# Performance work log

Hardware: AMD Instinct MI355X
Metric: run time of the kernel (lower is better)

Reference implementation:

```python
import jax, jax.numpy as jnp
import numpy as np

H = 256      # HIDDEN_DIM
F_IN = 16    # input_dim
B = 512
S = 168      # encoder sequence length
T = 24       # PRED_LEN


def _lstm_cell(x, h, c, w_ih, w_hh, b):
    # torch gate order: i, f, g, o
    g = x @ w_ih.T + h @ w_hh.T + b
    i, f, gg, o = jnp.split(g, 4, axis=-1)
    c_new = jax.nn.sigmoid(f) * c + jax.nn.sigmoid(i) * jnp.tanh(gg)
    h_new = jax.nn.sigmoid(o) * jnp.tanh(c_new)
    return h_new, c_new


def _lstm_layer(x, w_ih, w_hh, b):
    # x: [S, B, in] -> outputs [S, B, H], final (h, c)
    Bv, Hv = x.shape[1], w_hh.shape[1]
    init = (jnp.zeros((Bv, Hv), x.dtype), jnp.zeros((Bv, Hv), x.dtype))
    def step(carry, xt):
        h, c = _lstm_cell(xt, carry[0], carry[1], w_ih, w_hh, b)
        return (h, c), h
    (h, c), ys = jax.lax.scan(step, init, x)
    return ys, h, c


def setup_inputs() -> dict:
    key = jax.random.key(0)
    ks = jax.random.split(key, 24)
    s = 1.0 / np.sqrt(H)
    u = lambda k, shape: jax.random.uniform(k, shape, jnp.float32, -s, s)
    inp = {}
    inp['src'] = jax.random.normal(ks[0], (B, S, F_IN), jnp.float32)
    # encoder LSTM (2 layers); biases b_ih + b_hh fused into one vector
    inp['enc_w_ih0'] = u(ks[1], (4 * H, F_IN))
    inp['enc_w_hh0'] = u(ks[2], (4 * H, H))
    inp['enc_b0'] = u(ks[3], (4 * H,))
    inp['enc_w_ih1'] = u(ks[4], (4 * H, H))
    inp['enc_w_hh1'] = u(ks[5], (4 * H, H))
    inp['enc_b1'] = u(ks[6], (4 * H,))
    # decoder LSTM (2 layers), input_size = 1 + H
    inp['dec_w_ih0'] = u(ks[7], (4 * H, 1 + H))
    inp['dec_w_hh0'] = u(ks[8], (4 * H, H))
    inp['dec_b0'] = u(ks[9], (4 * H,))
    inp['dec_w_ih1'] = u(ks[10], (4 * H, H))
    inp['dec_w_hh1'] = u(ks[11], (4 * H, H))
    inp['dec_b1'] = u(ks[12], (4 * H,))
    # attention: Linear(2H -> H), v: Linear(H -> 1, no bias), position bias
    inp['attn_w'] = u(ks[13], (H, 2 * H))
    inp['attn_b'] = u(ks[14], (H,))
    inp['attn_v'] = u(ks[15], (H,))
    inp['pos_bias'] = jax.random.normal(ks[16], (H,), jnp.float32)
    # fc_out: Linear(H -> 1)
    inp['fc_w'] = u(ks[17], (1, H))
    inp['fc_b'] = u(ks[18], (1,))
    return inp


def reference(src, enc_w_ih0, enc_w_hh0, enc_b0, enc_w_ih1, enc_w_hh1, enc_b1,
              dec_w_ih0, dec_w_hh0, dec_b0, dec_w_ih1, dec_w_hh1, dec_b1,
              attn_w, attn_b, attn_v, pos_bias, fc_w, fc_b):
    x = jnp.transpose(src, (1, 0, 2))  # [S, B, F]
    y0, _, _ = _lstm_layer(x, enc_w_ih0, enc_w_hh0, enc_b0)
    enc_out_t, h1e, c1e = _lstm_layer(y0, enc_w_ih1, enc_w_hh1, enc_b1)
    # also need final state of layer 0 for decoder init
    h0e, c0e = y0[-1], None
    # recompute layer-0 final cell state: rerun scan carry output
    # (cheap alternative: _lstm_layer returns (ys, h, c); reuse it)
    _, h0e, c0e = _lstm_layer(x, enc_w_ih0, enc_w_hh0, enc_b0)
    enc_out = jnp.transpose(enc_out_t, (1, 0, 2))  # [B, S, H]

    We, Wd = attn_w[:, :H], attn_w[:, H:]
    enc_proj = jnp.einsum('bsh,gh->bsg', enc_out, We)  # precomputed encoder projection
    dec_in0 = src[:, -1, -1:]  # [B, 1]

    def dec_step(carry, t):
        h0, c0, h1, c1, dec_in = carry
        # additive attention using top-layer decoder hidden
        e = jnp.tanh(enc_proj + (h1 @ Wd.T + attn_b)[:, None, :])
        e = e + pos_bias[None, None, :] * (t / 24.0)
        w = jax.nn.softmax(e @ attn_v, axis=1)              # [B, S]
        ctx = jnp.einsum('bs,bsh->bh', w, enc_out)          # [B, H]
        x0 = jnp.concatenate([dec_in, ctx], axis=1)          # [B, 1+H]
        h0n, c0n = _lstm_cell(x0, h0, c0, dec_w_ih0, dec_w_hh0, dec_b0)
        h1n, c1n = _lstm_cell(h0n, h1, c1, dec_w_ih1, dec_w_hh1, dec_b1)
        pred = h1n @ fc_w.T + fc_b                           # [B, 1]
        # NOTE: the gated blend of decoder_output in the source is dead code
        # (the blended tensor is never used), so it is omitted here.
        return (h0n, c0n, h1n, c1n, pred), pred

    ts = jnp.arange(T, dtype=src.dtype)
    _, preds = jax.lax.scan(dec_step, (h0e, c0e, h1e, c1e, dec_in0), ts)
    return jnp.transpose(preds, (1, 0, 2))  # [B, T, 1]
```

## Files before the change

kernel.cpp:

```cpp
#include <hip/hip_runtime.h>
#include <hip/hip_fp16.h>
#include <math.h>

#define BB 512
#define HH 256
#define SS 168
#define TT 24
#define NBLK 256
#define NTHR 512
typedef unsigned long long ull;
typedef unsigned short u16;
#define BH 131072ull

#define O_Y0  0ull
#define O_H1  262144ull
#define O_H0  524288ull
#define O_CTX 786432ull
#define O_W0  933888ull
#define O_W1  1261568ull
#define O_WP  2834432ull
#define O_WDT 2835456ull
#define O_BP  2900992ull
#define O_E16 2905088ull
#define O_P16 13915136ull

typedef float f32x4 __attribute__((ext_vector_type(4)));
typedef float v2f __attribute__((ext_vector_type(2)));
typedef unsigned int ru4 __attribute__((ext_vector_type(4)));

__device__ __forceinline__ float sigf(float x) { return 1.f / (1.f + expf(-x)); }

#define AR __ATOMIC_RELAXED
#define SCA __HIP_MEMORY_SCOPE_AGENT
__device__ __forceinline__ int aLd(const int* p) { return __hip_atomic_load(p, AR, SCA); }

__device__ __forceinline__ float2 ld2(const float* p) {
  ull raw = __hip_atomic_load((const ull*)p, AR, SCA);
  float2 v; v.x = __uint_as_float((unsigned)raw); v.y = __uint_as_float((unsigned)(raw >> 32));
  return v;
}
__device__ __forceinline__ float ld1(const float* p) {
  unsigned raw = __hip_atomic_load((const unsigned*)p, AR, SCA);
  return __uint_as_float(raw);
}
__device__ __forceinline__ void st1(float* p, float v) {
  __hip_atomic_store((unsigned*)p, __float_as_uint(v), AR, SCA);
}
__device__ __forceinline__ void sth(__half* p, __half v) {
  __hip_atomic_store((unsigned short*)p, __half_as_ushort(v), AR, SCA);
}
__device__ __forceinline__ void stu(unsigned* p, unsigned v) {
  __hip_atomic_store(p, v, AR, SCA);
}

__device__ __forceinline__ void ld_h2(const float* p, v2f& a) {
  asm volatile("global_load_dwordx2 %0, %1, off sc0 sc1"
               : "=&v"(a) : "v"(p) : "memory");
}
__device__ __forceinline__ void ld_w2(const u16* ph, const u16* pl, ru4& h, ru4& l) {
  asm volatile("global_load_dwordx4 %0, %2, off\n\t"
               "global_load_dwordx4 %1, %3, off"
               : "=&v"(h), "=&v"(l) : "v"(ph), "v"(pl) : "memory");
}
#define VMW(n) asm volatile("s_waitcnt vmcnt(" #n ")" ::: "memory")

#define MFMA(d, a, b) asm volatile("v_mfma_f32_16x16x32_bf16 %0, %1, %2, %0" \
                                   : "+v"(d) : "v"(a), "v"(b))
#define TOUCH(x) asm volatile("" : "+v"(x))

#define SSTR 16
__device__ __forceinline__ void arrive_slot(int* slot, int val) {
  asm volatile("s_waitcnt vmcnt(0)" ::: "memory");
  __syncthreads();
  if (threadIdx.x == 0) __hip_atomic_store(slot, val, AR, SCA);
}
__device__ __forceinline__ void wait_slots(const int* base, int n, int tgt) {
  if (threadIdx.x < 64) {
    const int lane = threadIdx.x;
    const int* p = base + lane * SSTR;
    for (;;) {
      const int ok = (lane >= n) || (aLd(p) >= tgt);
      if (__all(ok)) break;
      __builtin_amdgcn_s_sleep(1);
    }
  }
  __syncthreads();
}
__device__ __forceinline__ void wait_slots2(const int* a, int na, const int* b, int nb, int tgt) {
  if (threadIdx.x < 64) {
    const int lane = threadIdx.x;
    const int* p = (lane < na) ? (a + lane * SSTR)
                 : (lane < na + nb) ? (b + (lane - na) * SSTR) : (const int*)nullptr;
    for (;;) {
      const int ok = (p == nullptr) || (aLd(p) >= tgt);
      if (__all(ok)) break;
      __builtin_amdgcn_s_sleep(1);
    }
  }
  __syncthreads();
}

struct SMT {
  union {
    struct { unsigned WsH[128][20]; unsigned WsL[128][20]; float Ht[32][36]; } m;
    struct { float As[32][65];  float Bs[32][65]; } g;
    struct { float h1s[256], qs[256], vs[256], sc[192], ctxs[1024], sred[4]; } at;
  };
};

__device__ __forceinline__ void fma16(float acc[4][4], const float4 hv, const float4 wv) {
  acc[0][0] += hv.x * wv.x; acc[0][1] += hv.x * wv.y; acc[0][2] += hv.x * wv.z; acc[0][3] += hv.x * wv.w;
  acc[1][0] += hv.y * wv.x; acc[1][1] += hv.y * wv.y; acc[1][2] += hv.y * wv.z; acc[1][3] += hv.y * wv.w;
  acc[2][0] += hv.z * wv.x; acc[2][1] += hv.z * wv.y; acc[2][2] += hv.z * wv.z; acc[2][3] += hv.z * wv.w;
  acc[3][0] += hv.w * wv.x; acc[3][1] += hv.w * wv.y; acc[3][2] += hv.w * wv.z; acc[3][3] += hv.w * wv.w;
}

__device__ __forceinline__ unsigned rne16(unsigned u) {
  return (u + 0x7fffu + ((u >> 16) & 1u)) >> 16;
}
__device__ __forceinline__ void split8v(const f32x4 a, const f32x4 b, ru4& hi, ru4& lo) {
#pragma unroll
  for (int j = 0; j < 4; j++) {
    const float x = (j < 2) ? a[2 * j] : b[2 * j - 4];
    const float y = (j < 2) ? a[2 * j + 1] : b[2 * j - 3];
    const unsigned hx = rne16(__float_as_uint(x)), hy = rne16(__float_as_uint(y));
    const float rx = x - __uint_as_float(hx << 16);
    const float ry = y - __uint_as_float(hy << 16);
    hi[j] = (hx & 0xffffu) | (hy << 16);
    lo[j] = (rne16(__float_as_uint(rx)) & 0xffffu) | (rne16(__float_as_uint(ry)) << 16);
  }
}

__device__ __forceinline__ void comp_mfma(SMT& sm, int wq, int w1, int l15, int l4,
                                          f32x4 acc[2])
{
  const int hr = w1 * 16 + l15;
  const f32x4 hv0 = *(const f32x4*)&sm.m.Ht[hr][l4 * 8];
  const f32x4 hv1 = *(const f32x4*)&sm.m.Ht[hr][l4 * 8 + 4];
  ru4 bhi, blo;
  split8v(hv0, hv1, bhi, blo);
  asm volatile("s_nop 1" : "+v"(bhi), "+v"(blo));
#pragma unroll
  for (int g = 0; g < 2; g++) {
    const int cr = wq * 32 + g * 16 + l15;
    ru4 ah = *(const ru4*)&sm.m.WsH[cr][l4 * 4];
    ru4 al = *(const ru4*)&sm.m.WsL[cr][l4 * 4];
    MFMA(acc[g], ah, bhi);
    MFMA(acc[g], ah, blo);
    MFMA(acc[g], al, bhi);
  }
}

#define STW(wh, wl) do { \
  *(ru4*)&sm.m.WsH[cgt][kt * 4] = (wh); \
  *(ru4*)&sm.m.WsL[cgt][kt * 4] = (wl); } while (0)
#define STH(a) do { \
  sm.m.Ht[r][p2 * 2] = (a)[0]; sm.m.Ht[r][p2 * 2 + 1] = (a)[1]; } while (0)

__device__ void gemm_pipe(const u16* wbh, const u16* wbl,
                          const float* hb0, const float* hb1,
                          int NC, int nc0, f32x4 acc[2], SMT& sm,
                          int wq, int w1, int l15, int l4)
{
  const int tid = threadIdx.x;
  const int r = tid & 31, p2 = tid >> 5;
  const int cgt = tid & 127, kt = tid >> 7;
  const float* h1p = hb1 - (ull)nc0 * 32;
#define HBk(k) (((k) < nc0) ? (hb0 + (k) * 32) : (h1p + (k) * 32))
  ru4 wh0, wl0, wh1, wl1, wh2, wl2, wh3, wl3;
  v2f h0, h1, h2, h3;
  ld_w2(wbh,      wbl,      wh0, wl0);
  ld_h2(HBk(0), h0);
  ld_w2(wbh + 32, wbl + 32, wh1, wl1);
  ld_h2(HBk(1), h1);
  ld_h2(HBk(2), h2);
  for (int c = 0; c < NC; c += 4) {
    VMW(4);
    STW(wh0, wl0); STH(h0);
    __syncthreads();
    ld_w2(wbh + (c + 2) * 32, wbl + (c + 2) * 32, wh2, wl2);
    ld_h2(HBk(c + 3), h3);
    comp_mfma(sm, wq, w1, l15, l4, acc);
    __syncthreads();
    VMW(4);
    STW(wh1, wl1); STH(h1);
    __syncthreads();
    ld_w2(wbh + (c + 3) * 32, wbl + (c + 3) * 32, wh3, wl3);
    ld_h2(HBk(c + 4), h0);
    comp_mfma(sm, wq, w1, l15, l4, acc);
    __syncthreads();
    VMW(4);
    STW(wh2, wl2); STH(h2);
    __syncthreads();
    ld_w2(wbh + (c + 4) * 32, wbl + (c + 4) * 32, wh0, wl0);
    ld_h2(HBk(c + 5), h1);
    comp_mfma(sm, wq, w1, l15, l4, acc);
    __syncthreads();
    VMW(4);
    STW(wh3, wl3); STH(h3);
    __syncthreads();
    ld_w2(wbh + (c + 5) * 32, wbl + (c + 5) * 32, wh1, wl1);
    ld_h2(HBk(c + 6), h2);
    comp_mfma(sm, wq, w1, l15, l4, acc);
    __syncthreads();
  }
  asm volatile("s_waitcnt vmcnt(0)" ::: "memory");
  asm volatile("s_nop 7\n\ts_nop 7" : "+v"(acc[0]), "+v"(acc[1]));
#undef HBk
}

__device__ __forceinline__ void lstm_epi2(f32x4 acc[2], float cR[2], int row, int ubase, int l4,
                                          float* hout, __half* e16, int sstep)
{
#pragma unroll
  for (int g = 0; g < 2; g++) {
    const int u = ubase + g * 4 + l4;
    const float iv = sigf(acc[g][0]), fv = sigf(acc[g][1]);
    const float gv = tanhf(acc[g][2]), ov = sigf(acc[g][3]);
    const float cn = fv * cR[g] + iv * gv;
    cR[g] = cn;
    const float hn = ov * tanhf(cn);
    st1(hout + (ull)row * 256 + u, hn);
    if (e16) sth(e16 + ((ull)row * SS + sstep) * 256 + u, __float2half(hn));
  }
}

__device__ void attn_fc(int row, int t, int slot, const float* h1r, const float* wdT,
                        const float* attn_b, const float* attn_v,
                        const __half* P16, const __half* E16,
                        const float* fc_w, const float* fc_b,
                        float* ctxb, float* out, SMT& sm)
{
  const int tid = threadIdx.x;
  __syncthreads();
  if (tid < 128) {
    float2 v = ld2(h1r + (ull)slot * BH + (ull)row * 256 + tid * 2);
    sm.at.h1s[tid * 2] = v.x; sm.at.h1s[tid * 2 + 1] = v.y;
  }
  __syncthreads();
  if (t >= 1 && tid < 64) {
    float a = 0.f;
#pragma unroll
    for (int j = 0; j < 4; j++) a += sm.at.h1s[tid + 64 * j] * fc_w[tid + 64 * j];
#pragma unroll
    for (int m = 32; m >= 1; m >>= 1) a += __shfl_xor(a, m, 64);
    if (tid == 0) {
      const float p = a + fc_b[0];
      out[(ull)row * TT + (t - 1)] = p;
      st1(ctxb + (ull)row * 288 + 256, p);
    }
  }
  if (t >= TT) return;
  if (tid < 256) {
    float qv = attn_b[tid];
    for (int k = 0; k < 256; k += 4) {
      qv += sm.at.h1s[k]     * wdT[(ull)(k)     * 256 + tid];
      qv += sm.at.h1s[k + 1] * wdT[(ull)(k + 1) * 256 + tid];
      qv += sm.at.h1s[k + 2] * wdT[(ull)(k + 2) * 256 + tid];
      qv += sm.at.h1s[k + 3] * wdT[(ull)(k + 3) * 256 + tid];
    }
    sm.at.qs[tid] = qv;
    sm.at.vs[tid] = attn_v[tid];
  }
  __syncthreads();
  const int wv = tid >> 6, lane = tid & 63;
  for (int s = wv; s < SS; s += 8) {
    const __half2* Pr = (const __half2*)(P16 + ((ull)row * SS + s) * 256);
    float a = 0.f;
#pragma unroll
    for (int jj = 0; jj < 2; jj++) {
      const int i2 = lane + 64 * jj;
      const float2 pv = __half22float2(Pr[i2]);
      const int g0 = i2 * 2;
      a += sm.at.vs[g0] * tanhf(pv.x + sm.at.qs[g0]);
      a += sm.at.vs[g0 + 1] * tanhf(pv.y + sm.at.qs[g0 + 1]);
    }
#pragma unroll
    for (int m = 32; m >= 1; m >>= 1) a += __shfl_xor(a, m, 64);
    if (lane == 0) sm.at.sc[s] = a;
  }
  __syncthreads();
  if (tid < 64) {
    float m = -1e30f;
    for (int i = tid; i < SS; i += 64) m = fmaxf(m, sm.at.sc[i]);
#pragma unroll
    for (int mm = 32; mm >= 1; mm >>= 1) m = fmaxf(m, __shfl_xor(m, mm, 64));
    if (tid == 0) sm.at.sred[0] = m;
  }
  __syncthreads();
  const float smax = sm.at.sred[0];
  if (tid < SS) sm.at.sc[tid] = expf(sm.at.sc[tid] - smax);
  __syncthreads();
  if (tid < 64) {
    float ssum = 0.f;
    for (int i = tid; i < SS; i += 64) ssum += sm.at.sc[i];
#pragma unroll
    for (int mm = 32; mm >= 1; mm >>= 1) ssum += __shfl_xor(ssum, mm, 64);
    if (tid == 0) sm.at.sred[1] = ssum;
  }
  __syncthreads();
  const float rinv = 1.f / sm.at.sred[1];
  const int u2 = tid & 127, sh = tid >> 7;
  float cx = 0.f, cy = 0.f;
  for (int s = sh * 42; s < sh * 42 + 42; s++) {
    const float w = sm.at.sc[s] * rinv;
    const float2 ev = __half22float2(*(const __half2*)(E16 + ((ull)row * SS + s) * 256 + u2 * 2));
    cx += w * ev.x; cy += w * ev.y;
  }
  sm.at.ctxs[sh * 256 + u2 * 2] = cx;
  sm.at.ctxs[sh * 256 + u2 * 2 + 1] = cy;
  __syncthreads();
  if (tid < 256)
    st1(ctxb + (ull)row * 288 + tid,
        sm.at.ctxs[tid] + sm.at.ctxs[256 + tid] + sm.at.ctxs[512 + tid] + sm.at.ctxs[768 + tid]);
}

__device__ void proj_tile(const __half* E16, const float* attn_w, __half* P16,
                          int m0, int n0, SMT& sm)
{
  const int tid = threadIdx.x;
  const bool act = tid < 256;
  const int mq = tid & 15, nq = (tid >> 4) & 15;
  const int li = tid & 63, kq = (tid >> 6) & 3;
  float acc[4][4] = {{0.f}};
  for (int k0 = 0; k0 < 256; k0 += 32) {
    if (act) {
      float4 raw = *(const float4*)(E16 + (ull)(m0 + li) * 256 + k0 + kq * 8);
      const __half* hp = (const __half*)&raw;
#pragma unroll
      for (int i = 0; i < 8; i++) sm.g.As[kq * 8 + i][li] = __half2float(hp[i]);
      const float* gb = attn_w + (ull)(n0 + li) * 512 + k0 + kq * 8;
      const float4 v0 = *(const float4*)gb, v1 = *(const float4*)(gb + 4);
      sm.g.Bs[kq * 8 + 0][li] = v0.x; sm.g.Bs[kq * 8 + 1][li] = v0.y;
      sm.g.Bs[kq * 8 + 2][li] = v0.z; sm.g.Bs[kq * 8 + 3][li] = v0.w;
      sm.g.Bs[kq * 8 + 4][li] = v1.x; sm.g.Bs[kq * 8 + 5][li] = v1.y;
      sm.g.Bs[kq * 8 + 6][li] = v1.z; sm.g.Bs[kq * 8 + 7][li] = v1.w;
    }
    __syncthreads();
    if (act) {
#pragma unroll 8
      for (int kk = 0; kk < 32; kk++) {
        const float4 a4 = *(const float4*)&sm.g.As[kk][mq * 4];
        const float4 b4 = *(const float4*)&sm.g.Bs[kk][nq * 4];
        fma16(acc, a4, b4);
      }
    }
    __syncthreads();
  }
  if (act) {
#pragma unroll
    for (int i = 0; i < 4; i++) {
      const int m = m0 + mq * 4 + i;
#pragma unroll
      for (int j = 0; j < 2; j++) {
        __half2 h2; h2.x = __float2half(acc[i][j * 2]); h2.y = __float2half(acc[i][j * 2 + 1]);
        stu((unsigned*)(P16 + (ull)m * 256 + n0 + nq * 4) + j, *(unsigned*)&h2);
      }
    }
  }
}

__global__ __launch_bounds__(512, 1) void seq2seq_pipe(
    const float* __restrict__ src,
    const float* __restrict__ attn_w, const float* __restrict__ attn_b,
    const float* __restrict__ attn_v,
    const float* __restrict__ fc_w, const float* __restrict__ fc_b,
    float* __restrict__ out, int* __restrict__ ib)
{
  __shared__ SMT sm;
  const int blk = blockIdx.x;
  const int tid = threadIdx.x;
  float* fb = (float*)ib + 65536;
  float* y0r  = fb + O_Y0;
  float* h1r  = fb + O_H1;
  float* h0r  = fb + O_H0;
  float* zb   = h0r + BH;
  float* ctxb = fb + O_CTX;
  const u16* whi0 = (const u16*)(fb + O_W0);
  const u16* wlo0 = whi0 + 1024ull * 320;
  const u16* whi1 = (const u16*)(fb + O_W1);
  const u16* wlo1 = whi1 + 1024ull * 512;
  const u16* dhi0 = whi1 + 2ull * 1024 * 512;
  const u16* dlo0 = whi1 + 3ull * 1024 * 512;
  const u16* dhi1 = whi1 + 4ull * 1024 * 512;
  const u16* dlo1 = whi1 + 5ull * 1024 * 512;
  const float* wp  = fb + O_WP;
  const float* wdT = fb + O_WDT;
  const float* bp  = fb + O_BP;
  __half* E16 = (__half*)(fb + O_E16);
  __half* P16 = (__half*)(fb + O_P16);
  const int g = blk >> 5, m = blk & 31;
  const int rowg = g * 64;
  int* gf = ib + g * 4096;
  int* f_e0 = gf;
  int* f_e1 = gf + 256;
  int* f_pr = gf + 512;
  int* f_a  = gf + 1024;
  int* f_h0 = gf + 1536;
  int* f_h1 = gf + 1792;

  const int lm = (m < 16) ? m : (m - 16);
  const int rh = lm & 1, gi = lm >> 1;
  const int row0 = rowg + rh * 32;
  const int gc0 = gi * 128;
  const int w = tid >> 6;
  const int l15 = tid & 15, l4 = (tid >> 4) & 3;
  const int w1 = w & 1, wq = w >> 1;
  const int gcw = gc0 + wq * 32;
  const int myrow = row0 + w1 * 16 + l15;
  const int ubase = gcw >> 2;
  const int r = tid & 31;
  const int cgt = tid & 127, kt = tid >> 7;

  int* my_enc_slot = (m < 16 ? f_e0 : f_e1) + (rh * 8 + gi) * SSTR;
  const int* e0h = f_e0 + rh * 8 * SSTR;
  const int* e1h = f_e1 + rh * 8 * SSTR;

  float cReg[2] = {0.f, 0.f};

  for (int t = 0; t <= SS; t++) {
    if (t) wait_slots2(e0h, 8, e1h, 8, t);
    if (m < 16) {
      if (t < SS) {
        f32x4 acc[2];
#pragma unroll
        for (int gg = 0; gg < 2; gg++) {
          acc[gg] = *(const f32x4*)(bp + gcw + gg * 16 + l4 * 4);
          TOUCH(acc[gg]);
        }
        {
          ru4 wxh, wxl;
          ld_w2(whi0 + (ull)(gc0 + cgt) * 320 + kt * 8,
                wlo0 + (ull)(gc0 + cgt) * 320 + kt * 8, wxh, wxl);
          VMW(0);
          *(ru4*)&sm.m.WsH[cgt][kt * 4] = wxh;
          *(ru4*)&sm.m.WsL[cgt][kt * 4] = wxl;
          const int f = tid >> 5;
          sm.m.Ht[r][f]      = src[((ull)(row0 + r) * SS + t) * 16 + f];
          sm.m.Ht[r][f + 16] = 0.f;
          __syncthreads();
          comp_mfma(sm, wq, w1, l15, l4, acc);
          __syncthreads();
        }
        const float* ysrc = (t == 0) ? zb : (y0r + (ull)((t + 1) & 1) * BH);
        const float* hb0 = ysrc + (ull)(row0 + r) * 256 + (tid >> 5) * 2;
        gemm_pipe(whi0 + (ull)(gc0 + cgt) * 320 + 32 + kt * 8,
                  wlo0 + (ull)(gc0 + cgt) * 320 + 32 + kt * 8,
                  hb0, hb0, 8, 8, acc, sm, wq, w1, l15, l4);
        lstm_epi2(acc, cReg, myrow, ubase, l4, y0r + (ull)(t & 1) * BH, nullptr, 0);
      }
    } else {
      if (t >= 1) {
        const int s = t - 1;
        f32x4 acc[2];
#pragma unroll
        for (int gg = 0; gg < 2; gg++) {
          acc[gg] = *(const f32x4*)(bp + 1024 + gcw + gg * 16 + l4 * 4);
          TOUCH(acc[gg]);
        }
        const float* ysrc = y0r + (ull)(s & 1) * BH;
        const float* hsrc = (s == 0) ? zb : (h1r + (ull)((s + 1) & 1) * BH);
        const float* hb0 = ysrc + (ull)(row0 + r) * 256 + (tid >> 5) * 2;
        const float* hb1 = hsrc + (ull)(row0 + r) * 256 + (tid >> 5) * 2;
        gemm_pipe(whi1 + (ull)(gc0 + cgt) * 512 + kt * 8,
                  wlo1 + (ull)(gc0 + cgt) * 512 + kt * 8,
                  hb0, hb1, 16, 8, acc, sm, wq, w1, l15, l4);
        lstm_epi2(acc, cReg, myrow, ubase, l4, h1r + (ull)(s & 1) * BH, E16, s);
      }
    }
    arrive_slot(my_enc_slot, t + 1);
  }

  wait_slots(f_e1, 16, SS + 1);
  {
    const int em0 = rowg * SS;
    for (int tau = m; tau < 672; tau += 32)
      proj_tile(E16, attn_w, P16, em0 + (tau >> 2) * 64, (tau & 3) * 64, sm);
  }
  arrive_slot(f_pr + m * SSTR, 1);

  for (int t = 0; t <= TT; t++) {
    if (t == 0) wait_slots(f_pr, 32, 1);
    else wait_slots(f_h1, 16, t);
    const int slot = (t + 1) & 1;
    attn_fc(rowg + 2 * m,     t, slot, h1r, wdT, attn_b, attn_v, P16, E16, fc_w, fc_b, ctxb, out, sm);
    attn_fc(rowg + 2 * m + 1, t, slot, h1r, wdT, attn_b, attn_v, P16, E16, fc_w, fc_b, ctxb, out, sm);
    if (t == TT) break;
    arrive_slot(f_a + m * SSTR, t + 1);
    if (m < 16) {
      wait_slots(f_a, 32, t + 1);
      if (t) wait_slots(f_h0, 16, t);
      f32x4 acc[2];
#pragma unroll
      for (int gg = 0; gg < 2; gg++) {
        acc[gg] = *(const f32x4*)(bp + 2048 + gcw + gg * 16 + l4 * 4);
        TOUCH(acc[gg]);
      }
      const float* h0src = (t == 0) ? (y0r + BH) : (h0r + (ull)((t + 1) & 1) * BH);
      const float* hb0 = ctxb + (ull)(row0 + r) * 288 + (tid >> 5) * 2;
      const float* hb1 = h0src + (ull)(row0 + r) * 256 + (tid >> 5) * 2;
      gemm_pipe(dhi0 + (ull)(gc0 + cgt) * 512 + kt * 8,
                dlo0 + (ull)(gc0 + cgt) * 512 + kt * 8,
                hb0, hb1, 16, 8, acc, sm, wq, w1, l15, l4);
      const float p = ld1(ctxb + (ull)myrow * 288 + 256);
#pragma unroll
      for (int gg = 0; gg < 2; gg++) {
        const f32x4 wpv = *(const f32x4*)(wp + gcw + gg * 16 + l4 * 4);
        acc[gg] = acc[gg] + wpv * p;
      }
      lstm_epi2(acc, cReg, myrow, ubase, l4, h0r + (ull)(t & 1) * BH, nullptr, 0);
      arrive_slot(f_h0 + m * SSTR, t + 1);
    } else {
      wait_slots(f_h0, 16, t + 1);
      if (t) wait_slots(f_h1, 16, t);
      f32x4 acc[2];
#pragma unroll
      for (int gg = 0; gg < 2; gg++) {
        acc[gg] = *(const f32x4*)(bp + 3072 + gcw + gg * 16 + l4 * 4);
        TOUCH(acc[gg]);
      }
      const float* hb0 = h0r + (ull)(t & 1) * BH + (ull)(row0 + r) * 256 + (tid >> 5) * 2;
      const float* hb1 = h1r + (ull)((t + 1) & 1) * BH + (ull)(row0 + r) * 256 + (tid >> 5) * 2;
      gemm_pipe(dhi1 + (ull)(gc0 + cgt) * 512 + kt * 8,
                dlo1 + (ull)(gc0 + cgt) * 512 + kt * 8,
                hb0, hb1, 16, 8, acc, sm, wq, w1, l15, l4);
      lstm_epi2(acc, cReg, myrow, ubase, l4, h1r + (ull)(t & 1) * BH, nullptr, 0);
      arrive_slot(f_h1 + (m - 16) * SSTR, t + 1);
    }
  }
}

__device__ __forceinline__ void split_store(float v, u16* hi, u16* lo, ull i) {
  const unsigned u = __float_as_uint(v);
  const unsigned hb = (u + 0x7fffu + ((u >> 16) & 1u)) >> 16;
  const float rr = v - __uint_as_float(hb << 16);
  const unsigned ur = __float_as_uint(rr);
  const unsigned lb = (ur + 0x7fffu + ((ur >> 16) & 1u)) >> 16;
  hi[i] = (u16)hb; lo[i] = (u16)lb;
}

__global__ void init_all(
    const float* __restrict__ src,
    const float* __restrict__ ewih0, const float* __restrict__ ewhh0, const float* __restrict__ eb0,
    const float* __restrict__ ewih1, const float* __restrict__ ewhh1, const float* __restrict__ eb1,
    const float* __restrict__ dwih0, const float* __restrict__ dwhh0, const float* __restrict__ db0,
    const float* __restrict__ dwih1, const float* __restrict__ dwhh1, const float* __restrict__ db1,
    const float* __restrict__ attn_w, int* __restrict__ ib)
{
  const int gid = blockIdx.x * 256 + threadIdx.x;
  const int NG = 1024 * 256;
  float* fb = (float*)ib + 65536;
  u16* whi0 = (u16*)(fb + O_W0);
  u16* wlo0 = whi0 + 1024ull * 320;
  u16* whi1 = (u16*)(fb + O_W1);
  u16* wlo1 = whi1 + 1024ull * 512;
  u16* dhi0 = whi1 + 2ull * 1024 * 512;
  u16* dlo0 = whi1 + 3ull * 1024 * 512;
  u16* dhi1 = whi1 + 4ull * 1024 * 512;
  u16* dlo1 = whi1 + 5ull * 1024 * 512;
  float* wpd = fb + O_WP;

  for (int i = gid; i < 32768; i += NG) ib[i] = 0;
  for (int i = gid; i < (int)BH; i += NG) fb[O_H0 + BH + i] = 0.f;
  for (int i = gid; i < 1024 * 320; i += NG) {
    const int cg = i / 320, k = i - cg * 320, j = (cg & 3) * 256 + (cg >> 2);
    float v = 0.f;
    if (k < 16) v = ewih0[(ull)j * 16 + k];
    else if (k >= 32 && k < 288) v = ewhh0[(ull)j * 256 + (k - 32)];
    split_store(v, whi0, wlo0, i);
  }
  for (int i = gid; i < 1024 * 512; i += NG) {
    const int cg = i >> 9, k = i & 511, j = (cg & 3) * 256 + (cg >> 2);
    split_store((k < 256) ? ewih1[(ull)j * 256 + k] : ewhh1[(ull)j * 256 + k - 256], whi1, wlo1, i);
    split_store((k < 256) ? dwih0[(ull)j * 257 + 1 + k] : dwhh0[(ull)j * 256 + k - 256], dhi0, dlo0, i);
    split_store((k < 256) ? dwih1[(ull)j * 256 + k] : dwhh1[(ull)j * 256 + k - 256], dhi1, dlo1, i);
  }
  for (int i = gid; i < 1024; i += NG) {
    const int j = (i & 3) * 256 + (i >> 2);
    wpd[i] = dwih0[(ull)j * 257];
  }
  for (int i = gid; i < 256 * 256; i += NG) {
    const int k = i >> 8, gg = i & 255;
    fb[O_WDT + i] = attn_w[(ull)gg * 512 + 256 + k];
  }
  for (int i = gid; i < 4096; i += NG) {
    const int set = i >> 10, cg = i & 1023, j = (cg & 3) * 256 + (cg >> 2);
    const float* bsrc = (set == 0) ? eb0 : (set == 1) ? eb1 : (set == 2) ? db0 : db1;
    fb[O_BP + i] = bsrc[j];
  }
  for (int i = gid; i < 512; i += NG)
    fb[O_CTX + (ull)i * 288 + 256] = src[((ull)i * SS + 167) * 16 + 15];
}

extern "C" void kernel_launch(void* const* d_in, const int* in_sizes, int n_in,
                              void* d_out, int out_size, void* d_ws, size_t ws_size,
                              hipStream_t stream)
{
  const float* src    = (const float*)d_in[0];
  const float* ewih0  = (const float*)d_in[1];
  const float* ewhh0  = (const float*)d_in[2];
  const float* eb0    = (const float*)d_in[3];
  const float* ewih1  = (const float*)d_in[4];
  const float* ewhh1  = (const float*)d_in[5];
  const float* eb1    = (const float*)d_in[6];
  const float* dwih0  = (const float*)d_in[7];
  const float* dwhh0  = (const float*)d_in[8];
  const float* db0    = (const float*)d_in[9];
  const float* dwih1  = (const float*)d_in[10];
  const float* dwhh1  = (const float*)d_in[11];
  const float* db1    = (const float*)d_in[12];
  const float* attn_w = (const float*)d_in[13];
  const float* attn_b = (const float*)d_in[14];
  const float* attn_v = (const float*)d_in[15];
  const float* fc_w   = (const float*)d_in[17];
  const float* fc_b   = (const float*)d_in[18];
  float* out = (float*)d_out;
  int* ib    = (int*)d_ws;

  init_all<<<1024, 256, 0, stream>>>(src, ewih0, ewhh0, eb0, ewih1, ewhh1, eb1,
                                     dwih0, dwhh0, db0, dwih1, dwhh1, db1, attn_w, ib);

  void* args[] = {
    (void*)&src, (void*)&attn_w, (void*)&attn_b, (void*)&attn_v,
    (void*)&fc_w, (void*)&fc_b, (void*)&out, (void*)&ib,
  };
  hipError_t lerr = hipLaunchCooperativeKernel((const void*)seq2seq_pipe, dim3(NBLK), dim3(NTHR),
                                               args, 0, stream);
  if (lerr != hipSuccess) {
    hipLaunchKernelGGL(seq2seq_pipe, dim3(NBLK), dim3(NTHR), 0, stream,
                       src, attn_w, attn_b, attn_v, fc_w, fc_b, out, ib);
  }
}
```

Measured before the change: 6.599 ms.

## Split persistent pipeline kernel into encoder, projection, and decoder launches

Measured after the change: 6.721 ms. Within noise of the previous version (+1.9%).

```diff
diff --git a/kernel.cpp b/kernel.cpp
--- a/kernel.cpp
+++ b/kernel.cpp
@@ -360,12 +360,8 @@
   }
 }
 
-__global__ __launch_bounds__(512, 1) void seq2seq_pipe(
-    const float* __restrict__ src,
-    const float* __restrict__ attn_w, const float* __restrict__ attn_b,
-    const float* __restrict__ attn_v,
-    const float* __restrict__ fc_w, const float* __restrict__ fc_b,
-    float* __restrict__ out, int* __restrict__ ib)
+__global__ __launch_bounds__(512, 1) void seq2seq_enc(
+    const float* __restrict__ src, int* __restrict__ ib)
 {
   __shared__ SMT sm;
   const int blk = blockIdx.x;
@@ -375,29 +371,17 @@
   float* h1r  = fb + O_H1;
   float* h0r  = fb + O_H0;
   float* zb   = h0r + BH;
-  float* ctxb = fb + O_CTX;
   const u16* whi0 = (const u16*)(fb + O_W0);
   const u16* wlo0 = whi0 + 1024ull * 320;
   const u16* whi1 = (const u16*)(fb + O_W1);
   const u16* wlo1 = whi1 + 1024ull * 512;
-  const u16* dhi0 = whi1 + 2ull * 1024 * 512;
-  const u16* dlo0 = whi1 + 3ull * 1024 * 512;
-  const u16* dhi1 = whi1 + 4ull * 1024 * 512;
-  const u16* dlo1 = whi1 + 5ull * 1024 * 512;
-  const float* wp  = fb + O_WP;
-  const float* wdT = fb + O_WDT;
   const float* bp  = fb + O_BP;
   __half* E16 = (__half*)(fb + O_E16);
-  __half* P16 = (__half*)(fb + O_P16);
   const int g = blk >> 5, m = blk & 31;
   const int rowg = g * 64;
   int* gf = ib + g * 4096;
   int* f_e0 = gf;
   int* f_e1 = gf + 256;
-  int* f_pr = gf + 512;
-  int* f_a  = gf + 1024;
-  int* f_h0 = gf + 1536;
-  int* f_h1 = gf + 1792;
 
   const int lm = (m < 16) ? m : (m - 16);
   const int rh = lm & 1, gi = lm >> 1;
@@ -448,6 +432,10 @@
                   wlo0 + (ull)(gc0 + cgt) * 320 + 32 + kt * 8,
                   hb0, hb0, 8, 8, acc, sm, wq, w1, l15, l4);
         lstm_epi2(acc, cReg, myrow, ubase, l4, y0r + (ull)(t & 1) * BH, nullptr, 0);
+      } else {
+#pragma unroll
+        for (int gg = 0; gg < 2; gg++)
+          st1(y0r + (ull)myrow * 256 + ubase + gg * 4 + l4, cReg[gg]);
       }
     } else {
       if (t >= 1) {
@@ -467,21 +455,84 @@
                   hb0, hb1, 16, 8, acc, sm, wq, w1, l15, l4);
         lstm_epi2(acc, cReg, myrow, ubase, l4, h1r + (ull)(s & 1) * BH, E16, s);
       }
-    }
-    arrive_slot(my_enc_slot, t + 1);
-  }
-
-  wait_slots(f_e1, 16, SS + 1);
+      if (t == SS) {
+#pragma unroll
+        for (int gg = 0; gg < 2; gg++)
+          st1(zb + (ull)myrow * 256 + ubase + gg * 4 + l4, cReg[gg]);
+      }
+    }
+    if (t < SS) arrive_slot(my_enc_slot, t + 1);
+  }
+}
+
+__global__ __launch_bounds__(256, 1) void seq2seq_proj(
+    const float* __restrict__ attn_w, int* __restrict__ ib)
+{
+  __shared__ SMT sm;
+  const int blk = blockIdx.x;
+  float* fb = (float*)ib + 65536;
+  __half* E16 = (__half*)(fb + O_E16);
+  __half* P16 = (__half*)(fb + O_P16);
+  const int g = blk >> 5, m = blk & 31;
+  const int em0 = g * 64 * SS;
+  for (int tau = m; tau < 672; tau += 32)
+    proj_tile(E16, attn_w, P16, em0 + (tau >> 2) * 64, (tau & 3) * 64, sm);
+}
+
+__global__ __launch_bounds__(512, 1) void seq2seq_dec(
+    const float* __restrict__ attn_b, const float* __restrict__ attn_v,
+    const float* __restrict__ fc_w, const float* __restrict__ fc_b,
+    float* __restrict__ out, int* __restrict__ ib)
+{
+  __shared__ SMT sm;
+  const int blk = blockIdx.x;
+  const int tid = threadIdx.x;
+  float* fb = (float*)ib + 65536;
+  float* y0r  = fb + O_Y0;
+  float* h1r  = fb + O_H1;
+  float* h0r  = fb + O_H0;
+  float* zb   = h0r + BH;
+  float* ctxb = fb + O_CTX;
+  const u16* whi1 = (const u16*)(fb + O_W1);
+  const u16* dhi0 = whi1 + 2ull * 1024 * 512;
+  const u16* dlo0 = whi1 + 3ull * 1024 * 512;
+  const u16* dhi1 = whi1 + 4ull * 1024 * 512;
+  const u16* dlo1 = whi1 + 5ull * 1024 * 512;
+  const float* wp  = fb + O_WP;
+  const float* wdT = fb + O_WDT;
+  const float* bp  = fb + O_BP;
+  __half* E16 = (__half*)(fb + O_E16);
+  __half* P16 = (__half*)(fb + O_P16);
+  const int g = blk >> 5, m = blk & 31;
+  const int rowg = g * 64;
+  int* gf = ib + g * 4096;
+  int* f_a  = gf + 1024;
+  int* f_h0 = gf + 1536;
+  int* f_h1 = gf + 1792;
+
+  const int lm = (m < 16) ? m : (m - 16);
+  const int rh = lm & 1, gi = lm >> 1;
+  const int row0 = rowg + rh * 32;
+  const int gc0 = gi * 128;
+  const int w = tid >> 6;
+  const int l15 = tid & 15, l4 = (tid >> 4) & 3;
+  const int w1 = w & 1, wq = w >> 1;
+  const int gcw = gc0 + wq * 32;
+  const int myrow = row0 + w1 * 16 + l15;
+  const int ubase = gcw >> 2;
+  const int r = tid & 31;
+  const int cgt = tid & 127, kt = tid >> 7;
+
+  float cReg[2];
   {
-    const int em0 = rowg * SS;
-    for (int tau = m; tau < 672; tau += 32)
-      proj_tile(E16, attn_w, P16, em0 + (tau >> 2) * 64, (tau & 3) * 64, sm);
-  }
-  arrive_slot(f_pr + m * SSTR, 1);
+    const float* csrc = (m < 16) ? y0r : zb;
+#pragma unroll
+    for (int gg = 0; gg < 2; gg++)
+      cReg[gg] = ld1(csrc + (ull)myrow * 256 + ubase + gg * 4 + l4);
+  }
 
   for (int t = 0; t <= TT; t++) {
-    if (t == 0) wait_slots(f_pr, 32, 1);
-    else wait_slots(f_h1, 16, t);
+    if (t) wait_slots(f_h1, 16, t);
     const int slot = (t + 1) & 1;
     attn_fc(rowg + 2 * m,     t, slot, h1r, wdT, attn_b, attn_v, P16, E16, fc_w, fc_b, ctxb, out, sm);
     attn_fc(rowg + 2 * m + 1, t, slot, h1r, wdT, attn_b, attn_v, P16, E16, fc_w, fc_b, ctxb, out, sm);
@@ -620,14 +671,21 @@
   init_all<<<1024, 256, 0, stream>>>(src, ewih0, ewhh0, eb0, ewih1, ewhh1, eb1,
                                      dwih0, dwhh0, db0, dwih1, dwhh1, db1, attn_w, ib);
 
-  void* args[] = {
-    (void*)&src, (void*)&attn_w, (void*)&attn_b, (void*)&attn_v,
-    (void*)&fc_w, (void*)&fc_b, (void*)&out, (void*)&ib,
-  };
-  hipError_t lerr = hipLaunchCooperativeKernel((const void*)seq2seq_pipe, dim3(NBLK), dim3(NTHR),
-                                               args, 0, stream);
-  if (lerr != hipSuccess) {
-    hipLaunchKernelGGL(seq2seq_pipe, dim3(NBLK), dim3(NTHR), 0, stream,
-                       src, attn_w, attn_b, attn_v, fc_w, fc_b, out, ib);
-  }
-}
+  {
+    void* args[] = { (void*)&src, (void*)&ib };
+    hipError_t e = hipLaunchCooperativeKernel((const void*)seq2seq_enc,
+                                              dim3(NBLK), dim3(NTHR), args, 0, stream);
+    if (e != hipSuccess)
+      hipLaunchKernelGGL(seq2seq_enc, dim3(NBLK), dim3(NTHR), 0, stream, src, ib);
+  }
+  hipLaunchKernelGGL(seq2seq_proj, dim3(NBLK), dim3(256), 0, stream, attn_w, ib);
+  {
+    void* args[] = { (void*)&attn_b, (void*)&attn_v, (void*)&fc_w, (void*)&fc_b,
+                     (void*)&out, (void*)&ib };
+    hipError_t e = hipLaunchCooperativeKernel((const void*)seq2seq_dec,
+                                              dim3(NBLK), dim3(NTHR), args, 0, stream);
+    if (e != hipSuccess)
+      hipLaunchKernelGGL(seq2seq_dec, dim3(NBLK), dim3(NTHR), 0, stream,
+                         attn_b, attn_v, fc_w, fc_b, out, ib);
+  }
+}
```
